# Performance work log

Measured on AMD Instinct MI355X. Metric: run time of the kernel, lower is better.

Reference implementation:

```python
import jax, jax.numpy as jnp
import numpy as np
from jax import lax

D_MODEL = 1024
STATE_DIM = 32
GROUPS = 8
GROUP_DIM = D_MODEL // GROUPS
DT_MIN = 0.001
DT_MAX = 0.1
EPS = 1e-6


def setup_inputs() -> dict:
    key = jax.random.key(0)
    ks = jax.random.split(key, 6)
    B, T = 4, 4096
    u = jax.random.normal(ks[0], (B, T, D_MODEL), dtype=jnp.float32)
    state = jnp.zeros((B, GROUPS, STATE_DIM), dtype=jnp.float32)
    A_log = jax.random.normal(ks[1], (GROUPS, STATE_DIM), dtype=jnp.float32) * 0.02
    B_param = jax.random.normal(ks[2], (GROUPS, STATE_DIM, GROUP_DIM), dtype=jnp.float32) * 0.02
    C = jax.random.normal(ks[3], (GROUPS, GROUP_DIM, STATE_DIM), dtype=jnp.float32) * 0.02
    Dp = jnp.zeros((GROUPS, GROUP_DIM), dtype=jnp.float32)
    dt_logit = jnp.zeros((GROUPS,), dtype=jnp.float32)
    return {"u": u, "state": state, "A_log": A_log, "B_param": B_param,
            "C": C, "Dp": Dp, "dt_logit": dt_logit}


def reference(u, state, A_log, B_param, C, Dp, dt_logit):
    Bsz, T, Dm = u.shape
    A = -jax.nn.softplus(A_log)                                  # [G,N]
    dt = DT_MIN + (DT_MAX - DT_MIN) * jax.nn.sigmoid(dt_logit)   # [G]
    dt_g = dt[:, None]                                           # [G,1]
    Abar = jnp.exp(A * dt_g)                                     # [G,N]
    # (exp(A dt) - 1)/A, stable for small |A|
    frac = jnp.where(jnp.abs(A) > EPS, (Abar - 1.0) / A,
                     jnp.broadcast_to(dt_g, A.shape))            # [G,N]
    Bbar = frac[..., None] * B_param                             # [G,N,gd]

    u_g = u.reshape(Bsz, T, GROUPS, GROUP_DIM)                   # [B,T,G,gd]
    # precompute input injections for all timesteps, then scan the LTI recurrence
    Bu = jnp.einsum('btgi,gni->btgn', u_g, Bbar)                 # [B,T,G,N]
    Bu_t = jnp.moveaxis(Bu, 1, 0)                                # [T,B,G,N]

    def step(s, bu):
        s = s * Abar + bu                                        # [B,G,N]
        return s, s

    s_final, states = lax.scan(step, state, Bu_t)                # states: [T,B,G,N]
    Cs = jnp.einsum('tbgn,gdn->btgd', states, C)                 # [B,T,G,gd]
    y = (Cs + Dp * u_g).reshape(Bsz, T, Dm)                      # [B,T,D]
    return y, s_final
```

## Files before the change

### kernel.cpp

```cpp
#include <hip/hip_runtime.h>
#include <hip/hip_bf16.h>

#define DM 1024
#define SD 32
#define NG 8
#define GD 128
#define BS 4
#define TT 4096
#define CL 64
#define NC (TT/CL)

typedef __attribute__((ext_vector_type(8))) short short8;
typedef __attribute__((ext_vector_type(4))) float f32x4;

#define WS_POWA  0
#define WS_STL   65536
#define WS_CARRY (WS_STL + 8388608)
#define WS_PAL   (WS_CARRY + 262144)

__device__ __forceinline__ unsigned short f2bf(float f) {
  __hip_bfloat16 h = __float2bfloat16(f);
  return __builtin_bit_cast(unsigned short, h);
}
__device__ __forceinline__ float bf2f(unsigned short h) {
  return __uint_as_float(((unsigned)h) << 16);
}
__device__ __forceinline__ float softplus_f(float x) {
  return (x > 20.f) ? x : log1pf(expf(x));
}
__device__ __forceinline__ short8 pack8(float4 a, float4 b) {
  short8 h;
  h[0]=(short)f2bf(a.x); h[1]=(short)f2bf(a.y); h[2]=(short)f2bf(a.z); h[3]=(short)f2bf(a.w);
  h[4]=(short)f2bf(b.x); h[5]=(short)f2bf(b.y); h[6]=(short)f2bf(b.z); h[7]=(short)f2bf(b.w);
  return h;
}

__global__ __launch_bounds__(64) void ka_bu_scan(const float* __restrict__ u,
                                                 const float* __restrict__ A_log,
                                                 const float* __restrict__ B_param,
                                                 const float* __restrict__ dt_logit,
                                                 unsigned char* __restrict__ ws) {
  const int bx = blockIdx.x;
  const int g = bx & (NG - 1);
  const int c = (bx >> 3) & (NC - 1);
  const int b = bx >> 9;
  const int l = threadIdx.x;
  const int lr = l & 15, lh = l >> 4;

  const float dtg = 0.001f + 0.099f * (1.f / (1.f + expf(-dt_logit[g])));

  float fracv[2];
  #pragma unroll
  for (int nt = 0; nt < 2; ++nt) {
    int n = nt * 16 + lr;
    float A = -softplus_f(A_log[g * SD + n]);
    float a = expf(A * dtg);
    fracv[nt] = (fabsf(A) > 1e-6f) ? (a - 1.f) / A : dtg;
  }
  float a_scan;
  {
    float A = -softplus_f(A_log[g * SD + (l & 31)]);
    a_scan = expf(A * dtg);
  }

  const float* bp = B_param + (size_t)g * SD * GD;
  short8 bfr[4][2];
  #pragma unroll
  for (int kt = 0; kt < 4; ++kt)
    #pragma unroll
    for (int nt = 0; nt < 2; ++nt) {
      const float* p = bp + (size_t)(nt * 16 + lr) * GD + kt * 32 + lh * 8;
      float4 v0 = *(const float4*)p;
      float4 v1 = *(const float4*)(p + 4);
      float s = fracv[nt];
      v0.x*=s; v0.y*=s; v0.z*=s; v0.w*=s;
      v1.x*=s; v1.y*=s; v1.z*=s; v1.w*=s;
      bfr[kt][nt] = pack8(v0, v1);
    }

  const float* up = u + ((size_t)b * TT + (size_t)c * CL) * DM + g * GD;
  float4 ub[2][4][2];
  #pragma unroll
  for (int kt = 0; kt < 2; ++kt)
    #pragma unroll
    for (int m = 0; m < 4; ++m) {
      const float* p = up + (size_t)(m * 16 + lr) * DM + kt * 32 + lh * 8;
      ub[kt][m][0] = *(const float4*)p;
      ub[kt][m][1] = *(const float4*)(p + 4);
    }

  f32x4 acc[4][2];
  #pragma unroll
  for (int m = 0; m < 4; ++m)
    #pragma unroll
    for (int nt = 0; nt < 2; ++nt)
      #pragma unroll
      for (int j = 0; j < 4; ++j) acc[m][nt][j] = 0.f;

  #pragma unroll
  for (int kt = 0; kt < 4; ++kt) {
    short8 af[4];
    #pragma unroll
    for (int m = 0; m < 4; ++m)
      af[m] = pack8(ub[kt & 1][m][0], ub[kt & 1][m][1]);
    if (kt < 2) {
      #pragma unroll
      for (int m = 0; m < 4; ++m) {
        const float* p = up + (size_t)(m * 16 + lr) * DM + (kt + 2) * 32 + lh * 8;
        ub[kt & 1][m][0] = *(const float4*)p;
        ub[kt & 1][m][1] = *(const float4*)(p + 4);
      }
    }
    #pragma unroll
    for (int m = 0; m < 4; ++m)
      #pragma unroll
      for (int nt = 0; nt < 2; ++nt)
        acc[m][nt] = __builtin_amdgcn_mfma_f32_16x16x32_bf16(af[m], bfr[kt][nt], acc[m][nt], 0, 0, 0);
  }

  __shared__ __align__(16) float sBu[CL * 33];
  __shared__ __align__(16) unsigned short sSt[CL * SD];
  #pragma unroll
  for (int m = 0; m < 4; ++m)
    #pragma unroll
    for (int nt = 0; nt < 2; ++nt)
      #pragma unroll
      for (int j = 0; j < 4; ++j) {
        int t = m * 16 + lh * 4 + j;
        sBu[t * 33 + (nt * 16 + lr)] = acc[m][nt][j];
      }
  __syncthreads();

  float* carry = (float*)(ws + WS_CARRY);
  if (l < SD) {
    float s = 0.f;
    #pragma unroll
    for (int t = 0; t < CL; ++t) {
      s = fmaf(s, a_scan, sBu[t * 33 + l]);
      sSt[t * SD + l] = f2bf(s);
    }
    carry[((b * NG + g) * NC + c) * SD + l] = s;
  }
  __syncthreads();

  unsigned short* stg = (unsigned short*)(ws + WS_STL) + ((size_t)((b * NC + c) * NG + g)) * CL * SD;
  #pragma unroll
  for (int p = 0; p < 4; ++p) {
    int off = (p * 64 + l) * 8;
    *(short8*)(stg + off) = *(short8*)(sSt + off);
  }

  if (b == 0 && c == 0 && l < SD) {
    float* powA = (float*)(ws + WS_POWA);
    float* powAL = (float*)(ws + WS_PAL);
    float p = 1.f;
    #pragma unroll
    for (int t = 0; t < CL; ++t) {
      p *= a_scan;
      powA[(g * CL + t) * SD + l] = p;
    }
    float aL = p;
    float q = 1.f;
    #pragma unroll
    for (int j = 0; j < CL; ++j) {
      powAL[(g * CL + j) * SD + l] = q;
      q *= aL;
    }
  }
}

__global__ __launch_bounds__(128) void kb_y(const float* __restrict__ u,
                                            const float* __restrict__ state0,
                                            const float* __restrict__ C,
                                            const float* __restrict__ Dp,
                                            unsigned char* __restrict__ ws,
                                            float* __restrict__ y,
                                            float* __restrict__ sfin) {
  const int bx = blockIdx.x;
  const int g = bx & (NG - 1);
  const int c = (bx >> 3) & (NC - 1);
  const int b = bx >> 9;
  const int tid = threadIdx.x;
  const int w = tid >> 6;
  const int l = tid & 63;
  const int lr = l & 15, lh = l >> 4;
  const int n = l & 31;

  const float* powA = (const float*)(ws + WS_POWA) + g * CL * SD;
  const float* powAL = (const float*)(ws + WS_PAL) + g * CL * SD;
  const float* carry = (const float*)(ws + WS_CARRY) + (size_t)(b * NG + g) * NC * SD;
  const unsigned short* stg = (const unsigned short*)(ws + WS_STL) + ((size_t)((b * NC + c) * NG + g)) * CL * SD;

  __shared__ __align__(16) float sY[32 * 132];

  bool need_u;
  {
    float2 dpc = *(const float2*)(Dp + g * GD + l * 2);
    need_u = __ballot((dpc.x != 0.f) || (dpc.y != 0.f)) != 0ULL;
  }

  float p;
  {
    float a0 = 0.f, a1 = 0.f, a2 = 0.f, a3 = 0.f;
    int cc = 0;
    while (cc + 8 <= c) {
      float ca[8], wt[8];
      #pragma unroll
      for (int e = 0; e < 8; ++e) {
        ca[e] = carry[(cc + e) * SD + n];
        wt[e] = powAL[(c - 1 - cc - e) * SD + n];
      }
      a0 = fmaf(wt[0], ca[0], a0); a1 = fmaf(wt[1], ca[1], a1);
      a2 = fmaf(wt[2], ca[2], a2); a3 = fmaf(wt[3], ca[3], a3);
      a0 = fmaf(wt[4], ca[4], a0); a1 = fmaf(wt[5], ca[5], a1);
      a2 = fmaf(wt[6], ca[6], a2); a3 = fmaf(wt[7], ca[7], a3);
      cc += 8;
    }
    for (; cc < c; ++cc)
      a0 = fmaf(powAL[(c - 1 - cc) * SD + n], carry[cc * SD + n], a0);
    p = fmaf(state0[(b * NG + g) * SD + n], powAL[c * SD + n], (a0 + a1) + (a2 + a3));
  }
  if (w == 0 && c == NC - 1 && l < SD) {
    const float aL = powA[(CL - 1) * SD + l];
    sfin[(b * NG + g) * SD + l] = fmaf(p, aL, carry[(NC - 1) * SD + l]);
  }

  float pr[8];
  #pragma unroll
  for (int e = 0; e < 8; ++e) pr[e] = __shfl(p, lh * 8 + e);

  short8 sf[4];
  #pragma unroll
  for (int tt = 0; tt < 4; ++tt) {
    int t = tt * 16 + lr;
    short8 sl = *(const short8*)(stg + t * SD + lh * 8);
    const float* pw = powA + t * SD + lh * 8;
    float4 pw0 = *(const float4*)pw;
    float4 pw1 = *(const float4*)(pw + 4);
    short8 hh;
    hh[0] = (short)f2bf(bf2f((unsigned short)sl[0]) + pw0.x * pr[0]);
    hh[1] = (short)f2bf(bf2f((unsigned short)sl[1]) + pw0.y * pr[1]);
    hh[2] = (short)f2bf(bf2f((unsigned short)sl[2]) + pw0.z * pr[2]);
    hh[3] = (short)f2bf(bf2f((unsigned short)sl[3]) + pw0.w * pr[3]);
    hh[4] = (short)f2bf(bf2f((unsigned short)sl[4]) + pw1.x * pr[4]);
    hh[5] = (short)f2bf(bf2f((unsigned short)sl[5]) + pw1.y * pr[5]);
    hh[6] = (short)f2bf(bf2f((unsigned short)sl[6]) + pw1.z * pr[6]);
    hh[7] = (short)f2bf(bf2f((unsigned short)sl[7]) + pw1.w * pr[7]);
    sf[tt] = hh;
  }

  const float* cp = C + (size_t)g * GD * SD;
  const size_t rowbase = ((size_t)b * TT + (size_t)c * CL) * DM + g * GD;

  short8 cf[4];
  #pragma unroll
  for (int dd = 0; dd < 4; ++dd) {
    int d = (w * 4 + dd) * 16 + lr;
    const float* pp = cp + (size_t)d * SD + lh * 8;
    float4 v0 = *(const float4*)pp;
    float4 v1 = *(const float4*)(pp + 4);
    cf[dd] = pack8(v0, v1);
  }
  f32x4 acc[4][4];
  #pragma unroll
  for (int dd = 0; dd < 4; ++dd)
    #pragma unroll
    for (int tt = 0; tt < 4; ++tt) {
      f32x4 z;
      #pragma unroll
      for (int j = 0; j < 4; ++j) z[j] = 0.f;
      acc[dd][tt] = __builtin_amdgcn_mfma_f32_16x16x32_bf16(cf[dd], sf[tt], z, 0, 0, 0);
    }

  const int sd4 = (tid & 31) * 4;
  float4 dpv = *(const float4*)(Dp + g * GD + sd4);

  #pragma unroll
  for (int tp = 0; tp < 2; ++tp) {
    if (tp) __syncthreads();
    #pragma unroll
    for (int dd = 0; dd < 4; ++dd)
      #pragma unroll
      for (int q = 0; q < 2; ++q) {
        int tt = tp * 2 + q;
        int tl = q * 16 + lr;
        int d0 = (w * 4 + dd) * 16 + lh * 4;
        *(float4*)(sY + tl * 132 + d0) = (float4){acc[dd][tt][0], acc[dd][tt][1],
                                                  acc[dd][tt][2], acc[dd][tt][3]};
      }
    __syncthreads();
    #pragma unroll
    for (int r = 0; r < 8; ++r) {
      int tl = r * 4 + (tid >> 5);
      int t = tp * 32 + tl;
      float4 v = *(const float4*)(sY + tl * 132 + sd4);
      size_t off = rowbase + (size_t)t * DM + sd4;
      if (need_u) {
        float4 u4 = *(const float4*)(u + off);
        v.x += dpv.x * u4.x; v.y += dpv.y * u4.y;
        v.z += dpv.z * u4.z; v.w += dpv.w * u4.w;
      }
      *(float4*)(y + off) = v;
    }
  }
}

extern "C" void kernel_launch(void* const* d_in, const int* in_sizes, int n_in,
                              void* d_out, int out_size, void* d_ws, size_t ws_size,
                              hipStream_t stream) {
  const float* u       = (const float*)d_in[0];
  const float* state0  = (const float*)d_in[1];
  const float* A_log   = (const float*)d_in[2];
  const float* B_param = (const float*)d_in[3];
  const float* C       = (const float*)d_in[4];
  const float* Dp      = (const float*)d_in[5];
  const float* dtl     = (const float*)d_in[6];
  float* y = (float*)d_out;
  unsigned char* ws = (unsigned char*)d_ws;
  float* sfin = y + (size_t)BS * TT * DM;

  ka_bu_scan<<<dim3(BS * NG * NC), dim3(64), 0, stream>>>(u, A_log, B_param, dtl, ws);
  kb_y<<<dim3(BS * NG * NC), dim3(128), 0, stream>>>(u, state0, C, Dp, ws, y, sfin);
}
```

Baseline: 40.94 us.

## Compute chunk carry via weighted reduction and move intra-chunk scan into output kernel

The first kernel no longer runs a serial 64-step scan through shared memory. It computes each chunk's end state directly as a decay-weighted sum of the MFMA outputs using exp2 weights and cross-lane shuffles, then stores the raw Bu values in bf16 with a transposed layout. The second kernel now rebuilds per-chunk states with a sequential scan that starts from the prefix carry, which removes the powA table and the per-element correction. The intent is to drop a sync-heavy serial phase from kernel A. The cost is a 64-step serial scan on 32 threads in kernel B, plus bf16 rounding of Bu before the scan, which changes accuracy.

```diff
diff --git a/kernel.cpp b/kernel.cpp
--- a/kernel.cpp
+++ b/kernel.cpp
@@ -11,12 +11,12 @@
 #define NC (TT/CL)
 
 typedef __attribute__((ext_vector_type(8))) short short8;
+typedef __attribute__((ext_vector_type(4))) short short4v;
 typedef __attribute__((ext_vector_type(4))) float f32x4;
 
-#define WS_POWA  0
-#define WS_STL   65536
-#define WS_CARRY (WS_STL + 8388608)
-#define WS_PAL   (WS_CARRY + 262144)
+#define WS_PAL   0
+#define WS_BU    65536
+#define WS_CARRY (WS_BU + 8388608)
 
 __device__ __forceinline__ unsigned short f2bf(float f) {
   __hip_bfloat16 h = __float2bfloat16(f);
@@ -35,11 +35,11 @@
   return h;
 }
 
-__global__ __launch_bounds__(64) void ka_bu_scan(const float* __restrict__ u,
-                                                 const float* __restrict__ A_log,
-                                                 const float* __restrict__ B_param,
-                                                 const float* __restrict__ dt_logit,
-                                                 unsigned char* __restrict__ ws) {
+__global__ __launch_bounds__(64) void ka_bu(const float* __restrict__ u,
+                                            const float* __restrict__ A_log,
+                                            const float* __restrict__ B_param,
+                                            const float* __restrict__ dt_logit,
+                                            unsigned char* __restrict__ ws) {
   const int bx = blockIdx.x;
   const int g = bx & (NG - 1);
   const int c = (bx >> 3) & (NC - 1);
@@ -49,18 +49,14 @@
 
   const float dtg = 0.001f + 0.099f * (1.f / (1.f + expf(-dt_logit[g])));
 
-  float fracv[2];
+  float fracv[2], l2v[2];
   #pragma unroll
   for (int nt = 0; nt < 2; ++nt) {
-    int n = nt * 16 + lr;
-    float A = -softplus_f(A_log[g * SD + n]);
+    int np = nt * 16 + lr;
+    float A = -softplus_f(A_log[g * SD + np]);
     float a = expf(A * dtg);
     fracv[nt] = (fabsf(A) > 1e-6f) ? (a - 1.f) / A : dtg;
-  }
-  float a_scan;
-  {
-    float A = -softplus_f(A_log[g * SD + (l & 31)]);
-    a_scan = expf(A * dtg);
+    l2v[nt] = A * dtg * 1.44269504f;
   }
 
   const float* bp = B_param + (size_t)g * SD * GD;
@@ -118,48 +114,51 @@
         acc[m][nt] = __builtin_amdgcn_mfma_f32_16x16x32_bf16(af[m], bfr[kt][nt], acc[m][nt], 0, 0, 0);
   }
 
-  __shared__ __align__(16) float sBu[CL * 33];
-  __shared__ __align__(16) unsigned short sSt[CL * SD];
+  float part[2];
+  #pragma unroll
+  for (int nt = 0; nt < 2; ++nt) {
+    float r1 = exp2f(-l2v[nt]);
+    float pnt = 0.f;
+    #pragma unroll
+    for (int m = 0; m < 4; ++m) {
+      float wm = exp2f(l2v[nt] * (float)(63 - 16 * m - 4 * lh));
+      #pragma unroll
+      for (int j = 0; j < 4; ++j) {
+        pnt = fmaf(wm, acc[m][nt][j], pnt);
+        wm *= r1;
+      }
+    }
+    part[nt] = pnt;
+  }
+  #pragma unroll
+  for (int nt = 0; nt < 2; ++nt) {
+    part[nt] += __shfl_xor(part[nt], 16);
+    part[nt] += __shfl_xor(part[nt], 32);
+  }
+  float* carry = (float*)(ws + WS_CARRY);
+  if (l < 32)
+    carry[((size_t)(b * NG + g) * NC + c) * SD + l] = part[(l >> 4) & 1];
+
+  unsigned short* bu = (unsigned short*)(ws + WS_BU) + ((size_t)((b * NC + c) * NG + g)) * CL * SD;
   #pragma unroll
   for (int m = 0; m < 4; ++m)
     #pragma unroll
-    for (int nt = 0; nt < 2; ++nt)
-      #pragma unroll
-      for (int j = 0; j < 4; ++j) {
-        int t = m * 16 + lh * 4 + j;
-        sBu[t * 33 + (nt * 16 + lr)] = acc[m][nt][j];
-      }
-  __syncthreads();
-
-  float* carry = (float*)(ws + WS_CARRY);
-  if (l < SD) {
-    float s = 0.f;
-    #pragma unroll
-    for (int t = 0; t < CL; ++t) {
-      s = fmaf(s, a_scan, sBu[t * 33 + l]);
-      sSt[t * SD + l] = f2bf(s);
-    }
-    carry[((b * NG + g) * NC + c) * SD + l] = s;
-  }
-  __syncthreads();
-
-  unsigned short* stg = (unsigned short*)(ws + WS_STL) + ((size_t)((b * NC + c) * NG + g)) * CL * SD;
-  #pragma unroll
-  for (int p = 0; p < 4; ++p) {
-    int off = (p * 64 + l) * 8;
-    *(short8*)(stg + off) = *(short8*)(sSt + off);
-  }
+    for (int nt = 0; nt < 2; ++nt) {
+      short4v h4;
+      h4[0] = (short)f2bf(acc[m][nt][0]);
+      h4[1] = (short)f2bf(acc[m][nt][1]);
+      h4[2] = (short)f2bf(acc[m][nt][2]);
+      h4[3] = (short)f2bf(acc[m][nt][3]);
+      *(short4v*)(bu + (nt * 16 + lr) * CL + m * 16 + lh * 4) = h4;
+    }
 
   if (b == 0 && c == 0 && l < SD) {
-    float* powA = (float*)(ws + WS_POWA);
+    float A = -softplus_f(A_log[g * SD + l]);
+    float a = expf(A * dtg);
+    float aL = 1.f;
+    #pragma unroll
+    for (int t = 0; t < CL; ++t) aL *= a;
     float* powAL = (float*)(ws + WS_PAL);
-    float p = 1.f;
-    #pragma unroll
-    for (int t = 0; t < CL; ++t) {
-      p *= a_scan;
-      powA[(g * CL + t) * SD + l] = p;
-    }
-    float aL = p;
     float q = 1.f;
     #pragma unroll
     for (int j = 0; j < CL; ++j) {
@@ -171,8 +170,10 @@
 
 __global__ __launch_bounds__(128) void kb_y(const float* __restrict__ u,
                                             const float* __restrict__ state0,
+                                            const float* __restrict__ A_log,
                                             const float* __restrict__ C,
                                             const float* __restrict__ Dp,
+                                            const float* __restrict__ dt_logit,
                                             unsigned char* __restrict__ ws,
                                             float* __restrict__ y,
                                             float* __restrict__ sfin) {
@@ -186,18 +187,28 @@
   const int lr = l & 15, lh = l >> 4;
   const int n = l & 31;
 
-  const float* powA = (const float*)(ws + WS_POWA) + g * CL * SD;
   const float* powAL = (const float*)(ws + WS_PAL) + g * CL * SD;
   const float* carry = (const float*)(ws + WS_CARRY) + (size_t)(b * NG + g) * NC * SD;
-  const unsigned short* stg = (const unsigned short*)(ws + WS_STL) + ((size_t)((b * NC + c) * NG + g)) * CL * SD;
-
+  const unsigned short* bu = (const unsigned short*)(ws + WS_BU) + ((size_t)((b * NC + c) * NG + g)) * CL * SD;
+
+  __shared__ __align__(16) unsigned short sSt[CL * SD];
   __shared__ __align__(16) float sY[32 * 132];
+
+  short8 bu8[8];
+  if (tid < 32) {
+    #pragma unroll
+    for (int q = 0; q < 8; ++q)
+      bu8[q] = *(const short8*)(bu + tid * CL + q * 8);
+  }
 
   bool need_u;
   {
     float2 dpc = *(const float2*)(Dp + g * GD + l * 2);
     need_u = __ballot((dpc.x != 0.f) || (dpc.y != 0.f)) != 0ULL;
   }
+
+  const float dtg = 0.001f + 0.099f * (1.f / (1.f + expf(-dt_logit[g])));
+  const float a_n = expf(-softplus_f(A_log[g * SD + n]) * dtg);
 
   float p;
   {
@@ -221,33 +232,27 @@
     p = fmaf(state0[(b * NG + g) * SD + n], powAL[c * SD + n], (a0 + a1) + (a2 + a3));
   }
   if (w == 0 && c == NC - 1 && l < SD) {
-    const float aL = powA[(CL - 1) * SD + l];
+    const float aL = powAL[SD + l];
     sfin[(b * NG + g) * SD + l] = fmaf(p, aL, carry[(NC - 1) * SD + l]);
   }
 
-  float pr[8];
-  #pragma unroll
-  for (int e = 0; e < 8; ++e) pr[e] = __shfl(p, lh * 8 + e);
+  if (tid < 32) {
+    float s = p;
+    #pragma unroll
+    for (int q = 0; q < 8; ++q)
+      #pragma unroll
+      for (int e = 0; e < 8; ++e) {
+        int t = q * 8 + e;
+        s = fmaf(s, a_n, bf2f((unsigned short)bu8[q][e]));
+        sSt[t * SD + tid] = f2bf(s);
+      }
+  }
+  __syncthreads();
 
   short8 sf[4];
   #pragma unroll
-  for (int tt = 0; tt < 4; ++tt) {
-    int t = tt * 16 + lr;
-    short8 sl = *(const short8*)(stg + t * SD + lh * 8);
-    const float* pw = powA + t * SD + lh * 8;
-    float4 pw0 = *(const float4*)pw;
-    float4 pw1 = *(const float4*)(pw + 4);
-    short8 hh;
-    hh[0] = (short)f2bf(bf2f((unsigned short)sl[0]) + pw0.x * pr[0]);
-    hh[1] = (short)f2bf(bf2f((unsigned short)sl[1]) + pw0.y * pr[1]);
-    hh[2] = (short)f2bf(bf2f((unsigned short)sl[2]) + pw0.z * pr[2]);
-    hh[3] = (short)f2bf(bf2f((unsigned short)sl[3]) + pw0.w * pr[3]);
-    hh[4] = (short)f2bf(bf2f((unsigned short)sl[4]) + pw1.x * pr[4]);
-    hh[5] = (short)f2bf(bf2f((unsigned short)sl[5]) + pw1.y * pr[5]);
-    hh[6] = (short)f2bf(bf2f((unsigned short)sl[6]) + pw1.z * pr[6]);
-    hh[7] = (short)f2bf(bf2f((unsigned short)sl[7]) + pw1.w * pr[7]);
-    sf[tt] = hh;
-  }
+  for (int tt = 0; tt < 4; ++tt)
+    sf[tt] = *(const short8*)(sSt + (tt * 16 + lr) * SD + lh * 8);
 
   const float* cp = C + (size_t)g * GD * SD;
   const size_t rowbase = ((size_t)b * TT + (size_t)c * CL) * DM + g * GD;
@@ -319,6 +324,6 @@
   unsigned char* ws = (unsigned char*)d_ws;
   float* sfin = y + (size_t)BS * TT * DM;
 
-  ka_bu_scan<<<dim3(BS * NG * NC), dim3(64), 0, stream>>>(u, A_log, B_param, dtl, ws);
-  kb_y<<<dim3(BS * NG * NC), dim3(128), 0, stream>>>(u, state0, C, Dp, ws, y, sfin);
-}
+  ka_bu<<<dim3(BS * NG * NC), dim3(64), 0, stream>>>(u, A_log, B_param, dtl, ws);
+  kb_y<<<dim3(BS * NG * NC), dim3(128), 0, stream>>>(u, state0, A_log, C, Dp, dtl, ws, y, sfin);
+}
```

Result: no change. 41.45 us (+1.3%).
